# Optimization experiments

Measured on AMD Instinct MI355X. Metric: run time of the kernel, lower is better.

## Reference

```python
import jax, jax.numpy as jnp
import numpy as np

N = 100000      # nodes
E = 1600000     # edges (avg degree 16)
IN, H, H4, OUT = 2, 128, 32, 64
B = 1000        # batch_size for final view


def setup_inputs() -> dict:
    key = jax.random.key(0)
    ks = jax.random.split(key, 16)
    w = lambda k, s: (jax.random.normal(k, s, jnp.float32) * (1.0 / np.sqrt(s[0])))
    return {
        "x": jax.random.normal(ks[0], (N, IN), jnp.float32),
        "edge_index": jax.random.randint(ks[1], (2, E), 0, N, dtype=jnp.int32),
        "batch_size": B,
        "W1": w(ks[2], (IN, H)),  "b1": jnp.zeros((H,), jnp.float32),
        "W2": w(ks[3], (H, H)),   "b2": jnp.zeros((H,), jnp.float32),
        "W3": w(ks[4], (H, H4)),  "b3": jnp.zeros((H4,), jnp.float32),
        "W4": w(ks[5], (H4, H4)), "b4": jnp.zeros((H4,), jnp.float32),
        "W5": w(ks[6], (H4, OUT)),"b5": jnp.zeros((OUT,), jnp.float32),
        "Wl": w(ks[7], (OUT, 1)), "bl": jnp.zeros((1,), jnp.float32),
    }


def gcn_conv(x, src, dst, W, b, n):
    # PyG GCNConv: add self-loops, symmetric degree normalization, scatter-add.
    h = x @ W  # [N, F]
    deg = jax.ops.segment_sum(jnp.ones(src.shape[0], h.dtype), dst,
                              num_segments=n) + 1.0  # +1 for self-loop
    dinv = jax.lax.rsqrt(deg)  # deg >= 1, no inf
    norm = dinv[src] * dinv[dst]  # [E]
    agg = jax.ops.segment_sum(h[src] * norm[:, None], dst, num_segments=n)
    agg = agg + h * (dinv * dinv)[:, None]  # self-loop contribution
    return agg + b


def reference(x, edge_index, batch_size, W1, b1, W2, b2, W3, b3, W4, b4, W5, b5, Wl, bl):
    x = x.reshape(-1, 2)
    n = x.shape[0]
    src, dst = edge_index[0], edge_index[1]
    for W, b in ((W1, b1), (W2, b2), (W3, b3), (W4, b4), (W5, b5)):
        x = jax.nn.relu(gcn_conv(x, src, dst, W, b, n))
    x = x @ Wl + bl  # [N, 1]
    return x.reshape(batch_size, -1)
```

## Files before the change

kernel.cpp:

```cpp
#include <hip/hip_runtime.h>
#include <math.h>


static inline int cdiv(int a, int b) { return (a + b - 1) / b; }

__global__ void zero_i32(int* __restrict__ p, int n) {
    int i = blockIdx.x * 256 + threadIdx.x;
    if (i < n) p[i] = 0;
}

__global__ __launch_bounds__(256) void count_ranged(const int* __restrict__ dst,
                                                    int* __restrict__ cnt,
                                                    int E, int N, int echunk) {
    int cls = blockIdx.x & 7;
    int chunk = blockIdx.x >> 3;
    int per = (N + 7) >> 3;
    int lo = cls * per;
    int hi = lo + per; if (hi > N) hi = N;
    int e0 = chunk * echunk;
    int e1 = e0 + echunk; if (e1 > E) e1 = E;
    for (int e = e0 + (int)threadIdx.x; e < e1; e += 256) {
        int d = dst[e];
        if (d >= lo && d < hi) atomicAdd(&cnt[d], 1);
    }
}

__global__ void scan1(const int* __restrict__ cnt, int* __restrict__ off,
                      int* __restrict__ bsum, int n) {
    __shared__ int sm[256];
    int i = blockIdx.x * 256 + threadIdx.x;
    int v = (i < n) ? cnt[i] : 0;
    sm[threadIdx.x] = v;
    __syncthreads();
    for (int ofs = 1; ofs < 256; ofs <<= 1) {
        int t = (threadIdx.x >= (unsigned)ofs) ? sm[threadIdx.x - ofs] : 0;
        __syncthreads();
        sm[threadIdx.x] += t;
        __syncthreads();
    }
    if (i < n) off[i] = sm[threadIdx.x];
    if (threadIdx.x == 255) bsum[blockIdx.x] = sm[255];
}

__global__ void scan2(const int* __restrict__ bsum, int* __restrict__ bpre,
                      int nb, int* __restrict__ off, int N, int E) {
    __shared__ int sm[512];
    int t = threadIdx.x;
    sm[t] = (t < nb) ? bsum[t] : 0;
    __syncthreads();
    for (int ofs = 1; ofs < 512; ofs <<= 1) {
        int v = (t >= ofs) ? sm[t - ofs] : 0;
        __syncthreads();
        sm[t] += v;
        __syncthreads();
    }
    if (t < nb) bpre[t] = sm[t] - bsum[t];
    if (t == 0) off[N] = E;
}

__global__ void scan3_fused(const int* __restrict__ cnt, const int* __restrict__ bpre,
                            int* __restrict__ off, int* __restrict__ cursor,
                            const float* __restrict__ x, float* __restrict__ dinv,
                            float* __restrict__ xs, int n) {
    int i = blockIdx.x * 256 + threadIdx.x;
    if (i < n) {
        int c = cnt[i];
        int o = off[i] - c + bpre[blockIdx.x];
        off[i] = o;
        cursor[i] = o;
        float dv = 1.0f / sqrtf((float)c + 1.0f);
        dinv[i] = dv;
        float2 xv = *reinterpret_cast<const float2*>(x + 2 * (size_t)i);
        *reinterpret_cast<float2*>(xs + 2 * (size_t)i) = float2{dv * xv.x, dv * xv.y};
    }
}

__global__ __launch_bounds__(256) void fill_ranged(const int* __restrict__ src,
                                                   const int* __restrict__ dst,
                                                   int* __restrict__ cursor,
                                                   int* __restrict__ csr,
                                                   int E, int N, int echunk) {
    int cls = blockIdx.x & 7;
    int chunk = blockIdx.x >> 3;
    int per = (N + 7) >> 3;
    int lo = cls * per;
    int hi = lo + per; if (hi > N) hi = N;
    int e0 = chunk * echunk;
    int e1 = e0 + echunk; if (e1 > E) e1 = E;
    for (int e = e0 + (int)threadIdx.x; e < e1; e += 256) {
        int d = dst[e];
        if (d >= lo && d < hi) {
            int p = atomicAdd(&cursor[d], 1);
            csr[p] = src[e];
        }
    }
}

__global__ __launch_bounds__(256) void agg2_kernel(const float* __restrict__ xs,
                                                   const int* __restrict__ off,
                                                   const int* __restrict__ csr,
                                                   const float* __restrict__ dinv,
                                                   float* __restrict__ out, int n) {
    int v = blockIdx.x * 256 + threadIdx.x;
    if (v >= n) return;
    float a0 = 0.f, a1 = 0.f;
    int e0 = off[v], e1 = off[v + 1];
    for (int e = e0; e < e1; e++) {
        int s = csr[e];
        float2 q = *reinterpret_cast<const float2*>(xs + 2 * (size_t)s);
        a0 += q.x;
        a1 += q.y;
    }
    float dv = dinv[v];
    float2 xv = *reinterpret_cast<const float2*>(xs + 2 * (size_t)v);
    *reinterpret_cast<float2*>(out + 2 * (size_t)v) =
        float2{dv * (a0 + xv.x), dv * (a1 + xv.y)};
}

template <bool BR, bool PS>
__global__ __launch_bounds__(256) void agg128_kernel(const float* __restrict__ h,
                                                     const int* __restrict__ off,
                                                     const int* __restrict__ csr,
                                                     const float* __restrict__ dinv,
                                                     const float* __restrict__ bias,
                                                     float* __restrict__ out, int n) {
    int tid = threadIdx.x;
    int lane = tid & 63;
    int sl = lane & 15;
    int subbase = lane & ~15;
    int wave = tid >> 6;
    int v = blockIdx.x * 16 + wave * 4 + (lane >> 4);
    if (v >= n) return;

    int start = off[v];
    int end = off[v + 1];

    float4 accA = {0.f, 0.f, 0.f, 0.f};
    float4 accB = {0.f, 0.f, 0.f, 0.f};

    for (int base = start; base < end; base += 16) {
        int m = end - base;
        if (m > 16) m = 16;
        int idx = (sl < m) ? csr[base + sl] : 0;
        int i = 0;
        for (; i + 8 <= m; i += 8) {
            float4 ha[8], hb[8];
#pragma unroll
            for (int u = 0; u < 8; u++) {
                int s = __shfl(idx, subbase + i + u);
                const float* p = h + (size_t)s * 128 + sl * 8;
                ha[u] = *reinterpret_cast<const float4*>(p);
                hb[u] = *reinterpret_cast<const float4*>(p + 4);
            }
#pragma unroll
            for (int u = 0; u < 8; u++) {
                accA.x += ha[u].x; accA.y += ha[u].y; accA.z += ha[u].z; accA.w += ha[u].w;
                accB.x += hb[u].x; accB.y += hb[u].y; accB.z += hb[u].z; accB.w += hb[u].w;
            }
        }
        if (i + 4 <= m) {
            float4 ha[4], hb[4];
#pragma unroll
            for (int u = 0; u < 4; u++) {
                int s = __shfl(idx, subbase + i + u);
                const float* p = h + (size_t)s * 128 + sl * 8;
                ha[u] = *reinterpret_cast<const float4*>(p);
                hb[u] = *reinterpret_cast<const float4*>(p + 4);
            }
#pragma unroll
            for (int u = 0; u < 4; u++) {
                accA.x += ha[u].x; accA.y += ha[u].y; accA.z += ha[u].z; accA.w += ha[u].w;
                accB.x += hb[u].x; accB.y += hb[u].y; accB.z += hb[u].z; accB.w += hb[u].w;
            }
            i += 4;
        }
        if (i + 2 <= m) {
            int s0 = __shfl(idx, subbase + i);
            int s1 = __shfl(idx, subbase + i + 1);
            const float* p0 = h + (size_t)s0 * 128 + sl * 8;
            const float* p1 = h + (size_t)s1 * 128 + sl * 8;
            float4 a0 = *reinterpret_cast<const float4*>(p0);
            float4 b0 = *reinterpret_cast<const float4*>(p0 + 4);
            float4 a1 = *reinterpret_cast<const float4*>(p1);
            float4 b1 = *reinterpret_cast<const float4*>(p1 + 4);
            accA.x += a0.x + a1.x; accA.y += a0.y + a1.y;
            accA.z += a0.z + a1.z; accA.w += a0.w + a1.w;
            accB.x += b0.x + b1.x; accB.y += b0.y + b1.y;
            accB.z += b0.z + b1.z; accB.w += b0.w + b1.w;
            i += 2;
        }
        if (i < m) {
            int s0 = __shfl(idx, subbase + i);
            const float* p0 = h + (size_t)s0 * 128 + sl * 8;
            float4 a0 = *reinterpret_cast<const float4*>(p0);
            float4 b0 = *reinterpret_cast<const float4*>(p0 + 4);
            accA.x += a0.x; accA.y += a0.y; accA.z += a0.z; accA.w += a0.w;
            accB.x += b0.x; accB.y += b0.y; accB.z += b0.z; accB.w += b0.w;
        }
    }

    float dv = dinv[v];
    const float* pv = h + (size_t)v * 128 + sl * 8;
    float4 hvA = *reinterpret_cast<const float4*>(pv);
    float4 hvB = *reinterpret_cast<const float4*>(pv + 4);
    float4 oA, oB;
    oA.x = dv * (accA.x + hvA.x); oA.y = dv * (accA.y + hvA.y);
    oA.z = dv * (accA.z + hvA.z); oA.w = dv * (accA.w + hvA.w);
    oB.x = dv * (accB.x + hvB.x); oB.y = dv * (accB.y + hvB.y);
    oB.z = dv * (accB.z + hvB.z); oB.w = dv * (accB.w + hvB.w);
    if constexpr (BR) {
        float4 bA = *reinterpret_cast<const float4*>(bias + sl * 8);
        float4 bB = *reinterpret_cast<const float4*>(bias + sl * 8 + 4);
        oA.x = fmaxf(oA.x + bA.x, 0.f); oA.y = fmaxf(oA.y + bA.y, 0.f);
        oA.z = fmaxf(oA.z + bA.z, 0.f); oA.w = fmaxf(oA.w + bA.w, 0.f);
        oB.x = fmaxf(oB.x + bB.x, 0.f); oB.y = fmaxf(oB.y + bB.y, 0.f);
        oB.z = fmaxf(oB.z + bB.z, 0.f); oB.w = fmaxf(oB.w + bB.w, 0.f);
    }
    if constexpr (PS) {
        oA.x *= dv; oA.y *= dv; oA.z *= dv; oA.w *= dv;
        oB.x *= dv; oB.y *= dv; oB.z *= dv; oB.w *= dv;
    }
    float* po = out + (size_t)v * 128 + sl * 8;
    *reinterpret_cast<float4*>(po) = oA;
    *reinterpret_cast<float4*>(po + 4) = oB;
}

template <bool BR, bool PS>
__global__ __launch_bounds__(256) void agg32_kernel(const float* __restrict__ h,
                                                    const int* __restrict__ off,
                                                    const int* __restrict__ csr,
                                                    const float* __restrict__ dinv,
                                                    const float* __restrict__ bias,
                                                    float* __restrict__ out, int n) {
    int tid = threadIdx.x;
    int lane = tid & 63;
    int sl = lane & 7;
    int subbase = lane & ~7;
    int wave = tid >> 6;
    int v = blockIdx.x * 32 + wave * 8 + (lane >> 3);
    if (v >= n) return;

    int start = off[v];
    int end = off[v + 1];

    float4 acc = {0.f, 0.f, 0.f, 0.f};

    for (int base = start; base < end; base += 16) {
        int m = end - base;
        if (m > 16) m = 16;
        int idxA = (sl < m) ? csr[base + sl] : 0;
        int idxB = (8 + sl < m) ? csr[base + 8 + sl] : 0;
        if (m == 16) {
            float4 hb[16];
#pragma unroll
            for (int u = 0; u < 16; u++) {
                int s = __shfl((u < 8) ? idxA : idxB, subbase + (u & 7));
                hb[u] = *reinterpret_cast<const float4*>(h + (size_t)s * 32 + sl * 4);
            }
#pragma unroll
            for (int u = 0; u < 16; u++) {
                acc.x += hb[u].x; acc.y += hb[u].y; acc.z += hb[u].z; acc.w += hb[u].w;
            }
        } else {
            int ma = (m < 8) ? m : 8;
            int i = 0;
            for (; i + 4 <= ma; i += 4) {
                float4 hb[4];
#pragma unroll
                for (int u = 0; u < 4; u++) {
                    int s = __shfl(idxA, subbase + i + u);
                    hb[u] = *reinterpret_cast<const float4*>(h + (size_t)s * 32 + sl * 4);
                }
#pragma unroll
                for (int u = 0; u < 4; u++) {
                    acc.x += hb[u].x; acc.y += hb[u].y; acc.z += hb[u].z; acc.w += hb[u].w;
                }
            }
            if (i + 2 <= ma) {
                int s0 = __shfl(idxA, subbase + i);
                int s1 = __shfl(idxA, subbase + i + 1);
                float4 h0 = *reinterpret_cast<const float4*>(h + (size_t)s0 * 32 + sl * 4);
                float4 h1 = *reinterpret_cast<const float4*>(h + (size_t)s1 * 32 + sl * 4);
                acc.x += h0.x + h1.x; acc.y += h0.y + h1.y;
                acc.z += h0.z + h1.z; acc.w += h0.w + h1.w;
                i += 2;
            }
            if (i < ma) {
                int s0 = __shfl(idxA, subbase + i);
                float4 h0 = *reinterpret_cast<const float4*>(h + (size_t)s0 * 32 + sl * 4);
                acc.x += h0.x; acc.y += h0.y; acc.z += h0.z; acc.w += h0.w;
            }
            if (m > 8) {
                int mb = m - 8;
                int j = 0;
                for (; j + 4 <= mb; j += 4) {
                    float4 hb[4];
#pragma unroll
                    for (int u = 0; u < 4; u++) {
                        int s = __shfl(idxB, subbase + j + u);
                        hb[u] = *reinterpret_cast<const float4*>(h + (size_t)s * 32 + sl * 4);
                    }
#pragma unroll
                    for (int u = 0; u < 4; u++) {
                        acc.x += hb[u].x; acc.y += hb[u].y; acc.z += hb[u].z; acc.w += hb[u].w;
                    }
                }
                if (j + 2 <= mb) {
                    int s0 = __shfl(idxB, subbase + j);
                    int s1 = __shfl(idxB, subbase + j + 1);
                    float4 h0 = *reinterpret_cast<const float4*>(h + (size_t)s0 * 32 + sl * 4);
                    float4 h1 = *reinterpret_cast<const float4*>(h + (size_t)s1 * 32 + sl * 4);
                    acc.x += h0.x + h1.x; acc.y += h0.y + h1.y;
                    acc.z += h0.z + h1.z; acc.w += h0.w + h1.w;
                    j += 2;
                }
                if (j < mb) {
                    int s0 = __shfl(idxB, subbase + j);
                    float4 h0 = *reinterpret_cast<const float4*>(h + (size_t)s0 * 32 + sl * 4);
                    acc.x += h0.x; acc.y += h0.y; acc.z += h0.z; acc.w += h0.w;
                }
            }
        }
    }

    float dv = dinv[v];
    float4 hv = *reinterpret_cast<const float4*>(h + (size_t)v * 32 + sl * 4);
    float o0 = dv * (acc.x + hv.x);
    float o1 = dv * (acc.y + hv.y);
    float o2 = dv * (acc.z + hv.z);
    float o3 = dv * (acc.w + hv.w);
    if constexpr (BR) {
        float4 b = *reinterpret_cast<const float4*>(bias + sl * 4);
        o0 = fmaxf(o0 + b.x, 0.f);
        o1 = fmaxf(o1 + b.y, 0.f);
        o2 = fmaxf(o2 + b.z, 0.f);
        o3 = fmaxf(o3 + b.w, 0.f);
    }
    if constexpr (PS) {
        o0 *= dv; o1 *= dv; o2 *= dv; o3 *= dv;
    }
    *reinterpret_cast<float4*>(out + (size_t)v * 32 + sl * 4) = float4{o0, o1, o2, o3};
}

template <int K, int F, bool BR, bool PS>
__global__ __launch_bounds__(256, 4) void gemm_tiled(const float* __restrict__ x,
                                                     const float* __restrict__ W,
                                                     const float* __restrict__ bias,
                                                     const float* __restrict__ dinv,
                                                     float* __restrict__ h, int n) {
    constexpr int KC = 16;
    constexpr int KCP = 20;
    constexpr int ROWS = 64;
    constexpr int TPC = F / 4;
    constexpr int RT = 256 / TPC;
    constexpr int RPT = ROWS / RT;
    static_assert(K % KC == 0, "K must be a multiple of 16");

    __shared__ float Ws[KC * F];
    __shared__ float Xs[ROWS * KCP];

    const int tid = threadIdx.x;
    const int cb = (tid % TPC) * 4;
    const int tr = tid / TPC;
    const int row0 = blockIdx.x * ROWS;

    float acc[RPT][4];
#pragma unroll
    for (int r = 0; r < RPT; r++)
#pragma unroll
        for (int j = 0; j < 4; j++) acc[r][j] = 0.f;

#pragma unroll 1
    for (int k0 = 0; k0 < K; k0 += KC) {
        __syncthreads();
        {
            int r = tid >> 2;
            int kk = (tid & 3) * 4;
            int gr = row0 + r;
            float4 v = (gr < n)
                ? *reinterpret_cast<const float4*>(x + (size_t)gr * K + k0 + kk)
                : float4{0.f, 0.f, 0.f, 0.f};
            *reinterpret_cast<float4*>(&Xs[r * KCP + kk]) = v;
        }
        for (int i = tid; i < KC * F / 4; i += 256) {
            *reinterpret_cast<float4*>(&Ws[i * 4]) =
                *reinterpret_cast<const float4*>(W + (size_t)k0 * F + i * 4);
        }
        __syncthreads();

#pragma unroll
        for (int kk4 = 0; kk4 < KC; kk4 += 4) {
            float4 xr[RPT];
#pragma unroll
            for (int r = 0; r < RPT; r++)
                xr[r] = *reinterpret_cast<const float4*>(&Xs[(tr * RPT + r) * KCP + kk4]);
#pragma unroll
            for (int j = 0; j < 4; j++) {
                float4 w = *reinterpret_cast<const float4*>(&Ws[(kk4 + j) * F + cb]);
#pragma unroll
                for (int r = 0; r < RPT; r++) {
                    float xv = (j == 0) ? xr[r].x : (j == 1) ? xr[r].y
                             : (j == 2) ? xr[r].z : xr[r].w;
                    acc[r][0] += xv * w.x;
                    acc[r][1] += xv * w.y;
                    acc[r][2] += xv * w.z;
                    acc[r][3] += xv * w.w;
                }
            }
        }
    }

    float4 b = float4{0.f, 0.f, 0.f, 0.f};
    if constexpr (BR) b = *reinterpret_cast<const float4*>(bias + cb);
#pragma unroll
    for (int r = 0; r < RPT; r++) {
        int row = row0 + tr * RPT + r;
        if (row < n) {
            float o0 = acc[r][0], o1 = acc[r][1], o2 = acc[r][2], o3 = acc[r][3];
            if constexpr (BR) {
                o0 = fmaxf(o0 + b.x, 0.f);
                o1 = fmaxf(o1 + b.y, 0.f);
                o2 = fmaxf(o2 + b.z, 0.f);
                o3 = fmaxf(o3 + b.w, 0.f);
            }
            if constexpr (PS) {
                float dv = dinv[row];
                o0 *= dv; o1 *= dv; o2 *= dv; o3 *= dv;
            }
            *reinterpret_cast<float4*>(&h[(size_t)row * F + cb]) = float4{o0, o1, o2, o3};
        }
    }
}

__global__ __launch_bounds__(256, 4) void gemm_final(const float* __restrict__ x,
                                                     const float* __restrict__ W,
                                                     const float* __restrict__ bias,
                                                     const float* __restrict__ Wl,
                                                     const float* __restrict__ bl,
                                                     float* __restrict__ out, int n) {
    constexpr int K = 32, F = 64;
    constexpr int KC = 16;
    constexpr int KCP = 20;
    constexpr int ROWS = 64;
    constexpr int TPC = F / 4;
    constexpr int RT = 256 / TPC;
    constexpr int RPT = ROWS / RT;

    __shared__ float Ws[KC * F];
    __shared__ float Xs[ROWS * KCP];
    __shared__ float wl[F];

    const int tid = threadIdx.x;
    if (tid < F) wl[tid] = Wl[tid];
    const int cb = (tid % TPC) * 4;
    const int tr = tid / TPC;
    const int row0 = blockIdx.x * ROWS;

    float acc[RPT][4];
#pragma unroll
    for (int r = 0; r < RPT; r++)
#pragma unroll
        for (int j = 0; j < 4; j++) acc[r][j] = 0.f;

#pragma unroll 1
    for (int k0 = 0; k0 < K; k0 += KC) {
        __syncthreads();
        {
            int r = tid >> 2;
            int kk = (tid & 3) * 4;
            int gr = row0 + r;
            float4 v = (gr < n)
                ? *reinterpret_cast<const float4*>(x + (size_t)gr * K + k0 + kk)
                : float4{0.f, 0.f, 0.f, 0.f};
            *reinterpret_cast<float4*>(&Xs[r * KCP + kk]) = v;
        }
        for (int i = tid; i < KC * F / 4; i += 256) {
            *reinterpret_cast<float4*>(&Ws[i * 4]) =
                *reinterpret_cast<const float4*>(W + (size_t)k0 * F + i * 4);
        }
        __syncthreads();

#pragma unroll
        for (int kk4 = 0; kk4 < KC; kk4 += 4) {
            float4 xr[RPT];
#pragma unroll
            for (int r = 0; r < RPT; r++)
                xr[r] = *reinterpret_cast<const float4*>(&Xs[(tr * RPT + r) * KCP + kk4]);
#pragma unroll
            for (int j = 0; j < 4; j++) {
                float4 w = *reinterpret_cast<const float4*>(&Ws[(kk4 + j) * F + cb]);
#pragma unroll
                for (int r = 0; r < RPT; r++) {
                    float xv = (j == 0) ? xr[r].x : (j == 1) ? xr[r].y
                             : (j == 2) ? xr[r].z : xr[r].w;
                    acc[r][0] += xv * w.x;
                    acc[r][1] += xv * w.y;
                    acc[r][2] += xv * w.z;
                    acc[r][3] += xv * w.w;
                }
            }
        }
    }

    float4 b = *reinterpret_cast<const float4*>(bias + cb);
    float4 w = *reinterpret_cast<const float4*>(&wl[cb]);
    float blv = bl[0];
#pragma unroll
    for (int r = 0; r < RPT; r++) {
        int row = row0 + tr * RPT + r;
        float o0 = fmaxf(acc[r][0] + b.x, 0.f);
        float o1 = fmaxf(acc[r][1] + b.y, 0.f);
        float o2 = fmaxf(acc[r][2] + b.z, 0.f);
        float o3 = fmaxf(acc[r][3] + b.w, 0.f);
        float partial = o0 * w.x + o1 * w.y + o2 * w.z + o3 * w.w;
        partial += __shfl_xor(partial, 8, 16);
        partial += __shfl_xor(partial, 4, 16);
        partial += __shfl_xor(partial, 2, 16);
        partial += __shfl_xor(partial, 1, 16);
        if ((tid & 15) == 0 && row < n) out[row] = partial + blv;
    }
}

template <int K, int F, bool BR, bool PS>
__global__ __launch_bounds__(256, 4) void gemm_small(const float* __restrict__ x,
                                                     const float* __restrict__ W,
                                                     const float* __restrict__ bias,
                                                     const float* __restrict__ dinv,
                                                     float* __restrict__ h, int n) {
    constexpr int TPR = F / 4;
    constexpr int ROWS = 256 / TPR;
    __shared__ float Ws[K * F];
    for (int i = threadIdx.x; i < K * F; i += 256) Ws[i] = W[i];
    __syncthreads();

    int tid = threadIdx.x;
    int cb = (tid % TPR) * 4;
    int r = blockIdx.x * ROWS + tid / TPR;
    if (r >= n) return;

    const float* xr = x + (size_t)r * K;
    float a0 = 0.f, a1 = 0.f, a2 = 0.f, a3 = 0.f;
#pragma unroll
    for (int k = 0; k < K; k++) {
        float xv = xr[k];
        float4 w = *reinterpret_cast<const float4*>(&Ws[k * F + cb]);
        a0 += xv * w.x; a1 += xv * w.y; a2 += xv * w.z; a3 += xv * w.w;
    }
    if constexpr (BR) {
        float4 b = *reinterpret_cast<const float4*>(bias + cb);
        a0 = fmaxf(a0 + b.x, 0.f);
        a1 = fmaxf(a1 + b.y, 0.f);
        a2 = fmaxf(a2 + b.z, 0.f);
        a3 = fmaxf(a3 + b.w, 0.f);
    }
    if constexpr (PS) {
        float dv = dinv[r];
        a0 *= dv; a1 *= dv; a2 *= dv; a3 *= dv;
    }
    *reinterpret_cast<float4*>(&h[(size_t)r * F + cb]) = float4{a0, a1, a2, a3};
}

extern "C" void kernel_launch(void* const* d_in, const int* in_sizes, int n_in,
                              void* d_out, int out_size, void* d_ws, size_t ws_size,
                              hipStream_t stream) {
    const float* x = (const float*)d_in[0];
    const int* ei = (const int*)d_in[1];
    const float* W1 = (const float*)d_in[3];
    const float* b1 = (const float*)d_in[4];
    const float* W2 = (const float*)d_in[5];
    const float* b2 = (const float*)d_in[6];
    const float* W3 = (const float*)d_in[7];
    const float* b3 = (const float*)d_in[8];
    const float* W4 = (const float*)d_in[9];
    const float* b4 = (const float*)d_in[10];
    const float* W5 = (const float*)d_in[11];
    const float* b5 = (const float*)d_in[12];
    const float* Wl = (const float*)d_in[13];
    const float* bl = (const float*)d_in[14];

    const int N = in_sizes[0] / 2;
    const int E = in_sizes[1] / 2;
    const int* src = ei;
    const int* dst = ei + E;

    char* wp = (char*)d_ws;
    auto alloc = [&](size_t bytes) -> void* {
        void* p = wp;
        wp += ((bytes + 255) / 256) * 256;
        return p;
    };
    int* cnt = (int*)alloc((size_t)N * 4);
    int* off = (int*)alloc((size_t)(N + 1) * 4);
    int* cursor = (int*)alloc((size_t)N * 4);
    int* bsum = (int*)alloc(512 * 4);
    int* bpre = (int*)alloc(512 * 4);
    int* csr = (int*)alloc((size_t)E * 4);
    float* dinv = (float*)alloc((size_t)N * 4);
    float* xs2 = (float*)alloc((size_t)N * 2 * 4);
    float* t2 = (float*)alloc((size_t)N * 2 * 4);
    float* bufA = (float*)alloc((size_t)N * 128 * 4);
    float* bufB = (float*)alloc((size_t)N * 128 * 4);

    const int gN = cdiv(N, 256);
    const int nb = gN;
    const int gT = cdiv(N, 64);

    const int NCHUNK = 128;
    const int echunk = cdiv(E, NCHUNK);
    const int gR = 8 * NCHUNK;

    zero_i32<<<gN, 256, 0, stream>>>(cnt, N);
    count_ranged<<<gR, 256, 0, stream>>>(dst, cnt, E, N, echunk);
    scan1<<<nb, 256, 0, stream>>>(cnt, off, bsum, N);
    scan2<<<1, 512, 0, stream>>>(bsum, bpre, nb, off, N, E);
    scan3_fused<<<nb, 256, 0, stream>>>(cnt, bpre, off, cursor, x, dinv, xs2, N);
    fill_ranged<<<gR, 256, 0, stream>>>(src, dst, cursor, csr, E, N, echunk);

    agg2_kernel<<<gN, 256, 0, stream>>>(xs2, off, csr, dinv, t2, N);
    gemm_small<2, 128, true, true><<<cdiv(N, 8), 256, 0, stream>>>(t2, W1, b1, dinv, bufA, N);
    gemm_tiled<128, 128, false, false><<<gT, 256, 0, stream>>>(bufA, W2, nullptr, nullptr, bufB, N);
    agg128_kernel<true, true><<<cdiv(N, 16), 256, 0, stream>>>(bufB, off, csr, dinv, b2, bufA, N);
    gemm_tiled<128, 32, false, false><<<gT, 256, 0, stream>>>(bufA, W3, nullptr, nullptr, bufB, N);
    agg32_kernel<true, true><<<cdiv(N, 32), 256, 0, stream>>>(bufB, off, csr, dinv, b3, bufA, N);
    gemm_tiled<32, 32, false, false><<<gT, 256, 0, stream>>>(bufA, W4, nullptr, nullptr, bufB, N);
    agg32_kernel<true, true><<<cdiv(N, 32), 256, 0, stream>>>(bufB, off, csr, dinv, b4, bufA, N);
    agg32_kernel<false, false><<<cdiv(N, 32), 256, 0, stream>>>(bufA, off, csr, dinv, nullptr, bufB, N);
    gemm_final<<<gT, 256, 0, stream>>>(bufB, W5, b5, Wl, bl, (float*)d_out, N);
}
```

Measured before the change: 560.9 us.

## Simplify degree counting and double GEMM K-chunk to 32

Replaces the range-partitioned degree count, which scanned every edge eight times with each pass filtering to one slice of the node range, with a single pass that does one atomic per edge. It also raises the GEMM shared-memory K chunk from 16 to 32, halving the number of barrier-separated load phases. In gemm_final, where K is 32, the K loop is removed entirely. Trade-offs are more atomic contention spread across the whole cnt array, and more shared memory per block, which could lower occupancy.

```diff
diff --git a/kernel.cpp b/kernel.cpp
--- a/kernel.cpp
+++ b/kernel.cpp
@@ -9,20 +9,9 @@
     if (i < n) p[i] = 0;
 }
 
-__global__ __launch_bounds__(256) void count_ranged(const int* __restrict__ dst,
-                                                    int* __restrict__ cnt,
-                                                    int E, int N, int echunk) {
-    int cls = blockIdx.x & 7;
-    int chunk = blockIdx.x >> 3;
-    int per = (N + 7) >> 3;
-    int lo = cls * per;
-    int hi = lo + per; if (hi > N) hi = N;
-    int e0 = chunk * echunk;
-    int e1 = e0 + echunk; if (e1 > E) e1 = E;
-    for (int e = e0 + (int)threadIdx.x; e < e1; e += 256) {
-        int d = dst[e];
-        if (d >= lo && d < hi) atomicAdd(&cnt[d], 1);
-    }
+__global__ void count_kernel(const int* __restrict__ dst, int* __restrict__ cnt, int E) {
+    int e = blockIdx.x * 256 + threadIdx.x;
+    if (e < E) atomicAdd(&cnt[dst[e]], 1);
 }
 
 __global__ void scan1(const int* __restrict__ cnt, int* __restrict__ off,
@@ -348,13 +337,13 @@
                                                      const float* __restrict__ bias,
                                                      const float* __restrict__ dinv,
                                                      float* __restrict__ h, int n) {
-    constexpr int KC = 16;
-    constexpr int KCP = 20;
+    constexpr int KC = 32;
+    constexpr int KCP = 36;
     constexpr int ROWS = 64;
     constexpr int TPC = F / 4;
     constexpr int RT = 256 / TPC;
     constexpr int RPT = ROWS / RT;
-    static_assert(K % KC == 0, "K must be a multiple of 16");
+    static_assert(K % KC == 0, "K must be a multiple of 32");
 
     __shared__ float Ws[KC * F];
     __shared__ float Xs[ROWS * KCP];
@@ -375,12 +364,15 @@
         __syncthreads();
         {
             int r = tid >> 2;
-            int kk = (tid & 3) * 4;
+            int kk = (tid & 3) * 8;
             int gr = row0 + r;
-            float4 v = (gr < n)
-                ? *reinterpret_cast<const float4*>(x + (size_t)gr * K + k0 + kk)
-                : float4{0.f, 0.f, 0.f, 0.f};
-            *reinterpret_cast<float4*>(&Xs[r * KCP + kk]) = v;
+            float4 v0 = {0.f, 0.f, 0.f, 0.f}, v1 = {0.f, 0.f, 0.f, 0.f};
+            if (gr < n) {
+                v0 = *reinterpret_cast<const float4*>(x + (size_t)gr * K + k0 + kk);
+                v1 = *reinterpret_cast<const float4*>(x + (size_t)gr * K + k0 + kk + 4);
+            }
+            *reinterpret_cast<float4*>(&Xs[r * KCP + kk]) = v0;
+            *reinterpret_cast<float4*>(&Xs[r * KCP + kk + 4]) = v1;
         }
         for (int i = tid; i < KC * F / 4; i += 256) {
             *reinterpret_cast<float4*>(&Ws[i * 4]) =
@@ -388,7 +380,7 @@
         }
         __syncthreads();
 
-#pragma unroll
+#pragma unroll 4
         for (int kk4 = 0; kk4 < KC; kk4 += 4) {
             float4 xr[RPT];
 #pragma unroll
@@ -439,8 +431,8 @@
                                                      const float* __restrict__ bl,
                                                      float* __restrict__ out, int n) {
     constexpr int K = 32, F = 64;
-    constexpr int KC = 16;
-    constexpr int KCP = 20;
+    constexpr int KC = 32;
+    constexpr int KCP = 36;
     constexpr int ROWS = 64;
     constexpr int TPC = F / 4;
     constexpr int RT = 256 / TPC;
@@ -462,25 +454,26 @@
 #pragma unroll
         for (int j = 0; j < 4; j++) acc[r][j] = 0.f;
 
-#pragma unroll 1
-    for (int k0 = 0; k0 < K; k0 += KC) {
-        __syncthreads();
+    {
         {
             int r = tid >> 2;
-            int kk = (tid & 3) * 4;
+            int kk = (tid & 3) * 8;
             int gr = row0 + r;
-            float4 v = (gr < n)
-                ? *reinterpret_cast<const float4*>(x + (size_t)gr * K + k0 + kk)
-                : float4{0.f, 0.f, 0.f, 0.f};
-            *reinterpret_cast<float4*>(&Xs[r * KCP + kk]) = v;
+            float4 v0 = {0.f, 0.f, 0.f, 0.f}, v1 = {0.f, 0.f, 0.f, 0.f};
+            if (gr < n) {
+                v0 = *reinterpret_cast<const float4*>(x + (size_t)gr * K + kk);
+                v1 = *reinterpret_cast<const float4*>(x + (size_t)gr * K + kk + 4);
+            }
+            *reinterpret_cast<float4*>(&Xs[r * KCP + kk]) = v0;
+            *reinterpret_cast<float4*>(&Xs[r * KCP + kk + 4]) = v1;
         }
         for (int i = tid; i < KC * F / 4; i += 256) {
             *reinterpret_cast<float4*>(&Ws[i * 4]) =
-                *reinterpret_cast<const float4*>(W + (size_t)k0 * F + i * 4);
+                *reinterpret_cast<const float4*>(W + i * 4);
         }
         __syncthreads();
 
-#pragma unroll
+#pragma unroll 4
         for (int kk4 = 0; kk4 < KC; kk4 += 4) {
             float4 xr[RPT];
 #pragma unroll
@@ -602,6 +595,7 @@
     float* bufB = (float*)alloc((size_t)N * 128 * 4);
 
     const int gN = cdiv(N, 256);
+    const int gE = cdiv(E, 256);
     const int nb = gN;
     const int gT = cdiv(N, 64);
 
@@ -610,7 +604,7 @@
     const int gR = 8 * NCHUNK;
 
     zero_i32<<<gN, 256, 0, stream>>>(cnt, N);
-    count_ranged<<<gR, 256, 0, stream>>>(dst, cnt, E, N, echunk);
+    count_kernel<<<gE, 256, 0, stream>>>(dst, cnt, E);
     scan1<<<nb, 256, 0, stream>>>(cnt, off, bsum, N);
     scan2<<<1, 512, 0, stream>>>(bsum, bpre, nb, off, N, E);
     scan3_fused<<<nb, 256, 0, stream>>>(cnt, bpre, off, cursor, x, dinv, xs2, N);
```

New measurement: 559.4 us (median of 2 runs). About the same (-0.3%).
